# Kernel tuning notes

Measured on AMD Instinct MI355X. Metric: run time of the kernel, lower is better.

Reference implementation:

```python
import jax, jax.numpy as jnp
import numpy as np

B, C, H, W = 8, 512, 96, 96
CQ = 64  # in_places // scale
EPS = 1e-06


def setup_inputs() -> dict:
    key = jax.random.key(0)
    ks = jax.random.split(key, 4)
    x = jax.random.normal(ks[0], (B, C, H, W), dtype=jnp.float32)
    wq = jax.random.normal(ks[1], (CQ, C), dtype=jnp.float32) * (1.0 / np.sqrt(C))
    wk = jax.random.normal(ks[2], (CQ, C), dtype=jnp.float32) * (1.0 / np.sqrt(C))
    wv = jax.random.normal(ks[3], (C, C), dtype=jnp.float32) * (1.0 / np.sqrt(C))
    bq = jnp.zeros((CQ,), jnp.float32)
    bk = jnp.zeros((CQ,), jnp.float32)
    bv = jnp.zeros((C,), jnp.float32)
    gamma = jnp.ones((1,), jnp.float32)
    return {"x": x, "wq": wq, "bq": bq, "wk": wk, "bk": bk, "wv": wv, "bv": bv, "gamma": gamma}


def reference(x, wq, bq, wk, bk, wv, bv, gamma):
    b, c, h, w = x.shape
    n = h * w
    xf = x.reshape(b, c, n)  # [b, c, n]
    # 1x1 convs == per-position channel GEMMs
    Q = jnp.einsum('oc,bcn->bon', wq, xf) + bq[None, :, None]  # [b, cq, n]
    K = jnp.einsum('oc,bcn->bon', wk, xf) + bk[None, :, None]  # [b, cq, n]
    V = jnp.einsum('oc,bcn->bon', wv, xf) + bv[None, :, None]  # [b, c, n]
    # L2 normalize over channel dim (dim=-2), matching torch l2_norm (no eps)
    Q = Q / jnp.linalg.norm(Q, axis=1, keepdims=True)
    K = K / jnp.linalg.norm(K, axis=1, keepdims=True)
    Qt = jnp.transpose(Q, (0, 2, 1))  # [b, n, cq]
    # tailor_sum = 1 / (N + Q . (sum_n K + eps))
    k_sum = K.sum(axis=-1) + EPS  # [b, cq]
    tailor = 1.0 / (n + jnp.einsum('bnm,bm->bn', Qt, k_sum))  # [b, n]
    v_sum = V.sum(axis=-1)  # [b, c]
    matrix = jnp.einsum('bmn,bcn->bmc', K, V)  # [b, cq, c]
    matrix_sum = v_sum[:, :, None] + jnp.einsum('bnm,bmc->bcn', Qt, matrix)  # [b, c, n]
    weight_value = matrix_sum * tailor[:, None, :]  # [b, c, n]
    return x + gamma[0] * weight_value.reshape(b, c, h, w)
```

## Files before the change

### kernel.cpp

```cpp
#include <hip/hip_runtime.h>

#define NB 8
#define NC 512
#define NQ 64
#define NN 9216
#define FEPS 1e-6f

typedef __attribute__((ext_vector_type(8))) short s16x8;
typedef __attribute__((ext_vector_type(4))) float f32x4;

static const size_t OFF_Q    = 0;
static const size_t OFF_KT   = OFF_Q + (size_t)NB * NQ * NN;
static const size_t OFF_KSUM = OFF_KT + (size_t)NB * NQ * NN;
static const size_t OFF_XSUM = OFF_KSUM + (size_t)NB * NQ;
static const size_t OFF_M1   = OFF_XSUM + (size_t)NB * NC;
static const size_t OFF_M2   = OFF_M1 + (size_t)NB * NQ * NC;
static const size_t OFF_VSUM = OFF_M2 + (size_t)NB * NQ * NC;
static const size_t OFF_WB   = OFF_VSUM + (size_t)NB * NC;

__device__ __forceinline__ void load_lds16(const void* g, void* l) {
    __builtin_amdgcn_global_load_lds((const __attribute__((address_space(1))) void*)g,
                                     (__attribute__((address_space(3))) void*)l, 16, 0, 0);
}

__device__ __forceinline__ unsigned cvt_pk_bf16(float lo, float hi) {
    unsigned r;
    asm("v_cvt_pk_bf16_f32 %0, %1, %2" : "=v"(r) : "v"(lo), "v"(hi));
    return r;
}

__device__ __forceinline__ unsigned short f2bf(float f) {
    union { float f; unsigned u; } a; a.f = f;
    unsigned r = a.u + 0x7FFFu + ((a.u >> 16) & 1u);
    return (unsigned short)(r >> 16);
}

__global__ void prep_w_kernel(const float* __restrict__ wq, const float* __restrict__ wk,
                              unsigned short* __restrict__ Wb) {
    const int idx = blockIdx.x * 256 + threadIdx.x;
#pragma unroll
    for (int k = 0; k < 4; ++k) {
        const int f4 = idx + k * 4096;
        const float* src = (f4 < 8192) ? wq : wk;
        const float4 v = *(const float4*)&src[(size_t)(f4 & 8191) * 4];
        uint2 u;
        u.x = cvt_pk_bf16(v.x, v.y);
        u.y = cvt_pk_bf16(v.z, v.w);
        *(uint2*)&Wb[(size_t)f4 * 4] = u;
    }
}

__launch_bounds__(256, 3)
__global__ void qk_mfma_kernel(const float* __restrict__ x,
                               const unsigned short* __restrict__ Wb,
                               const float* __restrict__ bq, const float* __restrict__ bk,
                               unsigned short* __restrict__ Qtb, unsigned short* __restrict__ Ktb,
                               float* __restrict__ ksum) {
    __shared__ __align__(16) unsigned short WX[12672];
    __shared__ float ssqL[4][64];
    unsigned short* Ws = WX;
    unsigned short* Xs = WX + 8192;
    const int t = threadIdx.x;
    const int w = t >> 6, lane = t & 63;
    const int g = lane >> 4, i16 = lane & 15;
    const int b = blockIdx.y;
    const int n0 = blockIdx.x * 64;
    const int srow = (w << 3) + (lane >> 3);
    const int sslot = lane & 7;

    f32x4 acc[2][4];
#pragma unroll
    for (int rt = 0; rt < 2; ++rt)
#pragma unroll
        for (int ct = 0; ct < 4; ++ct) acc[rt][ct] = {0.f, 0.f, 0.f, 0.f};

#pragma unroll 1
    for (int kc = 0; kc < NC; kc += 64) {
#pragma unroll
        for (int q = 0; q < 4; ++q) {
            const int row = q * 32 + srow;
            load_lds16(Wb + (size_t)row * NC + kc + ((sslot ^ (row & 7)) << 3),
                       Ws + (q * 32 + (w << 3)) * 64);
        }
#pragma unroll
        for (int r = 0; r < 2; ++r) {
            const int idx = r * 256 + t;
            const int cp = idx >> 4;
            const int p4 = (idx & 15) << 2;
            const float* xp = &x[((size_t)b * NC + kc + 2 * cp) * NN + n0 + p4];
            const float4 v0 = *(const float4*)xp;
            const float4 v1 = *(const float4*)(xp + NN);
            const float* f0 = (const float*)&v0;
            const float* f1 = (const float*)&v1;
#pragma unroll
            for (int j = 0; j < 4; ++j) {
                const int pos = p4 + j;
                const unsigned u = cvt_pk_bf16(f0[j], f1[j]);
                *(unsigned*)&Xs[pos * 64 + ((2 * cp) ^ ((pos & 7) << 3))] = u;
            }
        }
        __syncthreads();
#pragma unroll
        for (int ks = 0; ks < 2; ++ks) {
            s16x8 af[2], bfr[4];
#pragma unroll
            for (int rt = 0; rt < 2; ++rt) {
                const int row = (w << 5) + (rt << 4) + i16;
                af[rt] = *(const s16x8*)&Ws[row * 64 + (((ks << 5) + (g << 3)) ^ ((row & 7) << 3))];
            }
#pragma unroll
            for (int ct = 0; ct < 4; ++ct) {
                const int row = (ct << 4) + i16;
                bfr[ct] = *(const s16x8*)&Xs[row * 64 + (((ks << 5) + (g << 3)) ^ ((row & 7) << 3))];
            }
#pragma unroll
            for (int rt = 0; rt < 2; ++rt)
#pragma unroll
                for (int ct = 0; ct < 4; ++ct)
                    acc[rt][ct] = __builtin_amdgcn_mfma_f32_16x16x32_bf16(af[rt], bfr[ct], acc[rt][ct], 0, 0, 0);
        }
        __syncthreads();
    }

    const bool isK = (w >= 2);
    const int obase = (w & 1) * 32;
    const float* bias = isK ? bk : bq;
    float bv[2][4];
#pragma unroll
    for (int rt = 0; rt < 2; ++rt)
#pragma unroll
        for (int reg = 0; reg < 4; ++reg)
            bv[rt][reg] = bias[obase + rt * 16 + 4 * g + reg];
#pragma unroll
    for (int rt = 0; rt < 2; ++rt)
#pragma unroll
        for (int ct = 0; ct < 4; ++ct)
#pragma unroll
            for (int reg = 0; reg < 4; ++reg) acc[rt][ct][reg] += bv[rt][reg];

    float sq[4];
#pragma unroll
    for (int ct = 0; ct < 4; ++ct) {
        float s = 0.f;
#pragma unroll
        for (int rt = 0; rt < 2; ++rt)
#pragma unroll
            for (int reg = 0; reg < 4; ++reg) s += acc[rt][ct][reg] * acc[rt][ct][reg];
        s += __shfl_xor(s, 16, 64);
        s += __shfl_xor(s, 32, 64);
        sq[ct] = s;
    }
    ssqL[w][lane] = sq[g];
    __syncthreads();
    const int pairw = (w >> 1) << 1;
    float inv[4];
#pragma unroll
    for (int ct = 0; ct < 4; ++ct) {
        const int p = ct * 16 + i16;
        inv[ct] = rsqrtf(ssqL[pairw][p] + ssqL[pairw + 1][p]);
    }
#pragma unroll
    for (int rt = 0; rt < 2; ++rt)
#pragma unroll
        for (int ct = 0; ct < 4; ++ct)
#pragma unroll
            for (int reg = 0; reg < 4; ++reg) acc[rt][ct][reg] *= inv[ct];

    unsigned short* epQb = WX;
    unsigned short* epK = WX + 8320;
    if (!isK) {
#pragma unroll
        for (int rt = 0; rt < 2; ++rt)
#pragma unroll
            for (int ct = 0; ct < 4; ++ct)
#pragma unroll
                for (int reg = 0; reg < 4; ++reg) {
                    const int o = w * 32 + rt * 16 + 4 * g + reg;
                    const int pos = ct * 16 + i16;
                    epQb[pos * 64 + (o ^ ((pos & 7) << 3))] = f2bf(acc[rt][ct][reg]);
                }
    } else {
#pragma unroll
        for (int rt = 0; rt < 2; ++rt)
#pragma unroll
            for (int reg = 0; reg < 4; ++reg) {
                float s = acc[rt][0][reg] + acc[rt][1][reg] + acc[rt][2][reg] + acc[rt][3][reg];
                s += __shfl_xor(s, 1, 64);
                s += __shfl_xor(s, 2, 64);
                s += __shfl_xor(s, 4, 64);
                s += __shfl_xor(s, 8, 64);
                if (i16 == 0) atomicAdd(&ksum[b * NQ + obase + rt * 16 + 4 * g + reg], s);
            }
#pragma unroll
        for (int rt = 0; rt < 2; ++rt)
#pragma unroll
            for (int ct = 0; ct < 4; ++ct)
#pragma unroll
                for (int reg = 0; reg < 4; ++reg)
                    epK[(obase + rt * 16 + 4 * g + reg) * 68 + ct * 16 + i16] = f2bf(acc[rt][ct][reg]);
    }
    __syncthreads();
    {
        const size_t base = ((size_t)b * NN + n0) * 64;
        const uint4* src = (const uint4*)epQb;
#pragma unroll
        for (int r = 0; r < 2; ++r) {
            const int idx = r * 256 + t;
            *(uint4*)&Qtb[base + (size_t)idx * 8] = src[idx];
        }
    }
#pragma unroll
    for (int r = 0; r < 2; ++r) {
        const int idx = r * 256 + t;
        const int o = idx >> 3, s8 = (idx & 7) * 8;
        uint4 pk;
        unsigned short* up = (unsigned short*)&pk;
#pragma unroll
        for (int j = 0; j < 8; ++j) up[j] = epK[o * 68 + s8 + j];
        *(uint4*)&Ktb[((size_t)b * NQ + o) * NN + n0 + s8] = pk;
    }
}

__launch_bounds__(256, 4)
__global__ void kxt_mfma_kernel(const float* __restrict__ x, const unsigned short* __restrict__ Ktb,
                                float* __restrict__ mat1, float* __restrict__ xsum) {
    __shared__ __align__(16) unsigned short Ks[64 * 64];
    __shared__ __align__(16) unsigned short Xs[64 * 64];
    const int t = threadIdx.x;
    const int w = t >> 6, lane = t & 63;
    const int g = lane >> 4, i16 = lane & 15;
    const int nch = blockIdx.x, ct0 = blockIdx.y, b = blockIdx.z;
    const int c0 = ct0 * 64;
    const int pbeg = nch * 576;
    const int srow = (w << 3) + (lane >> 3);
    const int sslot = lane & 7;

    f32x4 acc[4];
#pragma unroll
    for (int ct = 0; ct < 4; ++ct) acc[ct] = {0.f, 0.f, 0.f, 0.f};
    float xs4[4] = {0.f, 0.f, 0.f, 0.f};

#pragma unroll 1
    for (int p0 = pbeg; p0 < pbeg + 576; p0 += 64) {
#pragma unroll
        for (int q = 0; q < 2; ++q) {
            const int row = q * 32 + srow;
            load_lds16(Ktb + ((size_t)b * NQ + row) * NN + p0 + ((sslot ^ (row & 7)) << 3),
                       Ks + (q * 32 + (w << 3)) * 64);
        }
#pragma unroll
        for (int r = 0; r < 4; ++r) {
            const int idx = r * 256 + t;
            const int c = idx >> 4, n4 = (idx & 15) << 2;
            const float4 v = *(const float4*)&x[((size_t)b * NC + c0 + c) * NN + p0 + n4];
            xs4[r] += (v.x + v.y) + (v.z + v.w);
            uint2 u;
            u.x = cvt_pk_bf16(v.x, v.y);
            u.y = cvt_pk_bf16(v.z, v.w);
            *(uint2*)&Xs[c * 64 + (n4 ^ ((c & 7) << 3))] = u;
        }
        __syncthreads();
#pragma unroll
        for (int ks = 0; ks < 2; ++ks) {
            s16x8 a8, b8[4];
            {
                const int row = (w << 4) + i16;
                a8 = *(const s16x8*)&Ks[row * 64 + (((ks << 5) + (g << 3)) ^ ((row & 7) << 3))];
            }
#pragma unroll
            for (int ct = 0; ct < 4; ++ct) {
                const int row = (ct << 4) + i16;
                b8[ct] = *(const s16x8*)&Xs[row * 64 + (((ks << 5) + (g << 3)) ^ ((row & 7) << 3))];
            }
#pragma unroll
            for (int ct = 0; ct < 4; ++ct)
                acc[ct] = __builtin_amdgcn_mfma_f32_16x16x32_bf16(a8, b8[ct], acc[ct], 0, 0, 0);
        }
        __syncthreads();
    }
    const int ob = (w << 4) + 4 * g;
#pragma unroll
    for (int ct = 0; ct < 4; ++ct)
#pragma unroll
        for (int reg = 0; reg < 4; ++reg)
            atomicAdd(&mat1[((size_t)b * NQ + ob + reg) * NC + c0 + (ct << 4) + i16], acc[ct][reg]);
#pragma unroll
    for (int r = 0; r < 4; ++r) {
        float s = xs4[r];
        s += __shfl_xor(s, 1, 64);
        s += __shfl_xor(s, 2, 64);
        s += __shfl_xor(s, 4, 64);
        s += __shfl_xor(s, 8, 64);
        if (i16 == 0) atomicAdd(&xsum[b * NC + c0 + r * 16 + (t >> 4)], s);
    }
}

__launch_bounds__(256)
__global__ void mat2_kernel(const float* __restrict__ wv, const float* __restrict__ bv,
                            const float* __restrict__ mat1, const float* __restrict__ ksum,
                            const float* __restrict__ xsum,
                            unsigned short* __restrict__ m2bT, float* __restrict__ vsum) {
    __shared__ __align__(16) float m1s[64 * 68];
    __shared__ __align__(16) float wvs[64 * 68];
    const int t = threadIdx.x;
    const int tx = t & 15, ty = t >> 4;
    const int ct = blockIdx.x, b = blockIdx.y;
    const int co0 = ct * 64;
    if (t < 64) {
        const int co = co0 + t;
        float s = 0.f;
        for (int c = 0; c < NC; ++c) s += wv[(size_t)co * NC + c] * xsum[b * NC + c];
        vsum[b * NC + co] = s + (float)NN * bv[co];
    }
    float acc[4][4] = {{0.f}};
    for (int cc = 0; cc < NC; cc += 64) {
#pragma unroll 1
        for (int r = 0; r < 4; ++r) {
            const int idx = r * 256 + t;
            const int row = idx >> 4, a = (idx & 15) * 4;
            *(float4*)&m1s[row * 68 + a] = *(const float4*)&mat1[((size_t)b * NQ + row) * NC + cc + a];
            *(float4*)&wvs[row * 68 + a] = *(const float4*)&wv[(size_t)(co0 + row) * NC + cc + a];
        }
        __syncthreads();
#pragma unroll 8
        for (int c4 = 0; c4 < 16; ++c4) {
            float4 mr[4], wr[4];
#pragma unroll
            for (int jo = 0; jo < 4; ++jo) mr[jo] = *(const float4*)&m1s[(ty + 16 * jo) * 68 + c4 * 4];
#pragma unroll
            for (int jc = 0; jc < 4; ++jc) wr[jc] = *(const float4*)&wvs[(tx + 16 * jc) * 68 + c4 * 4];
#pragma unroll
            for (int jo = 0; jo < 4; ++jo)
#pragma unroll
                for (int jc = 0; jc < 4; ++jc)
                    acc[jo][jc] += mr[jo].x * wr[jc].x + mr[jo].y * wr[jc].y +
                                   mr[jo].z * wr[jc].z + mr[jo].w * wr[jc].w;
        }
        __syncthreads();
    }
#pragma unroll
    for (int jo = 0; jo < 4; ++jo) {
        const float ks = ksum[b * NQ + ty + 16 * jo];
        const int o = ty + 16 * jo;
#pragma unroll
        for (int jc = 0; jc < 4; ++jc) {
            const int co = co0 + tx + 16 * jc;
            m2bT[((size_t)b * NC + co) * NQ + (o ^ ((co & 7) << 3))] = f2bf(acc[jo][jc] + ks * bv[co]);
        }
    }
}

__launch_bounds__(256, 4)
__global__ void final_mfma_kernel(const float* __restrict__ x, const unsigned short* __restrict__ Qtb,
                                  const float* __restrict__ ksum, const unsigned short* __restrict__ m2bT,
                                  const float* __restrict__ vsum, const float* __restrict__ gamma,
                                  float* __restrict__ out) {
    __shared__ __align__(16) unsigned short Qs[64 * 64];
    __shared__ __align__(16) unsigned short Ms[2][64 * 64];
    __shared__ float vsall[512];
    __shared__ float ksl[64];
    __shared__ float tl[64];
    const int t = threadIdx.x;
    const int w = t >> 6, lane = t & 63;
    const int g = lane >> 4, i16 = lane & 15;
    const int b = blockIdx.y;
    const int n0 = blockIdx.x * 64;

    const unsigned short* qg = Qtb + ((size_t)b * NN + n0) * 64;
    const unsigned short* mg = m2bT + (size_t)b * NC * 64;
#pragma unroll
    for (int r = 0; r < 2; ++r) {
        const int off = (w * 2 + r) * 512;
        load_lds16(qg + off + lane * 8, Qs + off);
        load_lds16(mg + off + lane * 8, &Ms[0][off]);
    }
    vsall[t] = vsum[b * NC + t];
    vsall[256 + t] = vsum[b * NC + 256 + t];
    if (t < 64) ksl[t] = ksum[b * NQ + t] + FEPS;
    __syncthreads();
    if (t < 64) {
        float s = 0.f;
        const int sw = (t & 7) << 3;
#pragma unroll 8
        for (int o = 0; o < 64; ++o) {
            union { unsigned u; float f; } cv;
            cv.u = (unsigned)Qs[t * 64 + o] << 16;
            s += cv.f * ksl[o ^ sw];
        }
        tl[t] = 1.0f / ((float)NN + s);
    }
    s16x8 af[4][2];
#pragma unroll
    for (int mt = 0; mt < 4; ++mt)
#pragma unroll
        for (int ks = 0; ks < 2; ++ks) {
            const int row = mt * 16 + i16;
            af[mt][ks] = *(const s16x8*)&Qs[row * 64 + (((ks << 5) + (g << 3)) ^ ((row & 7) << 3))];
        }
    const float gm = gamma[0];
    const int c_local = w * 16 + i16;
    __syncthreads();

#pragma unroll 1
    for (int cc8 = 0; cc8 < 8; ++cc8) {
        if (cc8 < 7) {
#pragma unroll
            for (int r = 0; r < 2; ++r) {
                const int off = (w * 2 + r) * 512;
                load_lds16(mg + (cc8 + 1) * 4096 + off + lane * 8, &Ms[(cc8 + 1) & 1][off]);
            }
        }
        const unsigned short* mbuf = Ms[cc8 & 1];
        s16x8 b8[2];
#pragma unroll
        for (int ks = 0; ks < 2; ++ks)
            b8[ks] = *(const s16x8*)&mbuf[c_local * 64 + (((ks << 5) + (g << 3)) ^ ((i16 & 7) << 3))];
        f32x4 acc[4];
#pragma unroll
        for (int mt = 0; mt < 4; ++mt) acc[mt] = {0.f, 0.f, 0.f, 0.f};
#pragma unroll
        for (int ks = 0; ks < 2; ++ks)
#pragma unroll
            for (int mt = 0; mt < 4; ++mt)
                acc[mt] = __builtin_amdgcn_mfma_f32_16x16x32_bf16(af[mt][ks], b8[ks], acc[mt], 0, 0, 0);
        const int c = cc8 * 64 + c_local;
        const float vsv = vsall[c];
        const size_t rowbase = ((size_t)b * NC + c) * NN + n0;
#pragma unroll
        for (int mt = 0; mt < 4; ++mt) {
            const int p = mt * 16 + 4 * g;
            const float4 xv = *(const float4*)&x[rowbase + p];
            const float4 t4 = *(const float4*)&tl[p];
            float4 ov;
            ov.x = xv.x + gm * (vsv + acc[mt][0]) * t4.x;
            ov.y = xv.y + gm * (vsv + acc[mt][1]) * t4.y;
            ov.z = xv.z + gm * (vsv + acc[mt][2]) * t4.z;
            ov.w = xv.w + gm * (vsv + acc[mt][3]) * t4.w;
            *(float4*)&out[rowbase + p] = ov;
        }
        __syncthreads();
    }
}

extern "C" void kernel_launch(void* const* d_in, const int* in_sizes, int n_in,
                              void* d_out, int out_size, void* d_ws, size_t ws_size,
                              hipStream_t stream) {
    (void)in_sizes; (void)n_in; (void)out_size; (void)ws_size;
    const float* x     = (const float*)d_in[0];
    const float* wq    = (const float*)d_in[1];
    const float* bq    = (const float*)d_in[2];
    const float* wk    = (const float*)d_in[3];
    const float* bk    = (const float*)d_in[4];
    const float* wv    = (const float*)d_in[5];
    const float* bv    = (const float*)d_in[6];
    const float* gamma = (const float*)d_in[7];
    float* out = (float*)d_out;
    float* ws  = (float*)d_ws;

    unsigned short* Qtb  = (unsigned short*)(ws + OFF_Q);
    unsigned short* Ktb  = (unsigned short*)(ws + OFF_KT);
    float* ksum          = ws + OFF_KSUM;
    float* xsum          = ws + OFF_XSUM;
    float* m1            = ws + OFF_M1;
    unsigned short* m2b  = (unsigned short*)(ws + OFF_M2);
    float* vsum          = ws + OFF_VSUM;
    unsigned short* Wb   = (unsigned short*)(ws + OFF_WB);

    hipMemsetAsync(ksum, 0, (size_t)(NB * NQ + NB * NC + NB * NQ * NC) * sizeof(float), stream);

    prep_w_kernel<<<dim3(16), 256, 0, stream>>>(wq, wk, Wb);
    qk_mfma_kernel<<<dim3(NN / 64, NB), 256, 0, stream>>>(x, Wb, bq, bk, Qtb, Ktb, ksum);
    kxt_mfma_kernel<<<dim3(16, 8, NB), 256, 0, stream>>>(x, Ktb, m1, xsum);
    mat2_kernel<<<dim3(8, NB), 256, 0, stream>>>(wv, bv, m1, ksum, xsum, m2b, vsum);
    final_mfma_kernel<<<dim3(NN / 64, NB), 256, 0, stream>>>(x, Qtb, ksum, m2b, vsum, gamma, out);
}
```

Baseline: 436.7 us.

## Fuse K^T·X product into QK kernel and use MFMA for Wv·mat1

The K·Xᵀ accumulation (mat1) and the x channel sums move into the QK projection kernel. Each block multiplies its freshly normalized K tile, kept in LDS, against bf16-converted x tiles and atomically adds the result into mat1, so the Ktb round trip through global memory and the separate kxt kernel go away. The mat2 GEMM is rewritten to use bf16 MFMA with Wv pre-converted to bf16 in the prep kernel. The cost is a second full read of x inside the QK kernel and far more global atomics on mat1, one set per 64-position block instead of per 576-position chunk, which may cause contention.

```diff
diff --git a/kernel.cpp b/kernel.cpp
--- a/kernel.cpp
+++ b/kernel.cpp
@@ -36,17 +36,31 @@
 }
 
 __global__ void prep_w_kernel(const float* __restrict__ wq, const float* __restrict__ wk,
-                              unsigned short* __restrict__ Wb) {
-    const int idx = blockIdx.x * 256 + threadIdx.x;
-#pragma unroll
-    for (int k = 0; k < 4; ++k) {
-        const int f4 = idx + k * 4096;
-        const float* src = (f4 < 8192) ? wq : wk;
-        const float4 v = *(const float4*)&src[(size_t)(f4 & 8191) * 4];
-        uint2 u;
-        u.x = cvt_pk_bf16(v.x, v.y);
-        u.y = cvt_pk_bf16(v.z, v.w);
-        *(uint2*)&Wb[(size_t)f4 * 4] = u;
+                              const float* __restrict__ wv,
+                              unsigned short* __restrict__ Wb, unsigned short* __restrict__ Wvb) {
+    if (blockIdx.x < 16) {
+        const int idx = blockIdx.x * 256 + threadIdx.x;
+#pragma unroll
+        for (int k = 0; k < 4; ++k) {
+            const int f4 = idx + k * 4096;
+            const float* src = (f4 < 8192) ? wq : wk;
+            const float4 v = *(const float4*)&src[(size_t)(f4 & 8191) * 4];
+            uint2 u;
+            u.x = cvt_pk_bf16(v.x, v.y);
+            u.y = cvt_pk_bf16(v.z, v.w);
+            *(uint2*)&Wb[(size_t)f4 * 4] = u;
+        }
+    } else {
+        const int idx = (blockIdx.x - 16) * 256 + threadIdx.x;
+#pragma unroll
+        for (int k = 0; k < 4; ++k) {
+            const int f4 = idx + k * 16384;
+            const float4 v = *(const float4*)&wv[(size_t)f4 * 4];
+            uint2 u;
+            u.x = cvt_pk_bf16(v.x, v.y);
+            u.y = cvt_pk_bf16(v.z, v.w);
+            *(uint2*)&Wvb[(size_t)f4 * 4] = u;
+        }
     }
 }
 
@@ -54,8 +68,9 @@
 __global__ void qk_mfma_kernel(const float* __restrict__ x,
                                const unsigned short* __restrict__ Wb,
                                const float* __restrict__ bq, const float* __restrict__ bk,
-                               unsigned short* __restrict__ Qtb, unsigned short* __restrict__ Ktb,
-                               float* __restrict__ ksum) {
+                               unsigned short* __restrict__ Qtb,
+                               float* __restrict__ ksum, float* __restrict__ xsum,
+                               float* __restrict__ mat1) {
     __shared__ __align__(16) unsigned short WX[12672];
     __shared__ float ssqL[4][64];
     unsigned short* Ws = WX;
@@ -167,7 +182,8 @@
             for (int reg = 0; reg < 4; ++reg) acc[rt][ct][reg] *= inv[ct];
 
     unsigned short* epQb = WX;
-    unsigned short* epK = WX + 8320;
+    unsigned short* epK  = WX + 8192;
+    unsigned short* xb   = WX + 4096;
     if (!isK) {
 #pragma unroll
         for (int rt = 0; rt < 2; ++rt)
@@ -196,8 +212,11 @@
 #pragma unroll
             for (int ct = 0; ct < 4; ++ct)
 #pragma unroll
-                for (int reg = 0; reg < 4; ++reg)
-                    epK[(obase + rt * 16 + 4 * g + reg) * 68 + ct * 16 + i16] = f2bf(acc[rt][ct][reg]);
+                for (int reg = 0; reg < 4; ++reg) {
+                    const int o = obase + rt * 16 + 4 * g + reg;
+                    const int pos = ct * 16 + i16;
+                    epK[o * 64 + (pos ^ ((o & 7) << 3))] = f2bf(acc[rt][ct][reg]);
+                }
     }
     __syncthreads();
     {
@@ -209,145 +228,137 @@
             *(uint4*)&Qtb[base + (size_t)idx * 8] = src[idx];
         }
     }
-#pragma unroll
-    for (int r = 0; r < 2; ++r) {
-        const int idx = r * 256 + t;
-        const int o = idx >> 3, s8 = (idx & 7) * 8;
-        uint4 pk;
-        unsigned short* up = (unsigned short*)&pk;
-#pragma unroll
-        for (int j = 0; j < 8; ++j) up[j] = epK[o * 68 + s8 + j];
-        *(uint4*)&Ktb[((size_t)b * NQ + o) * NN + n0 + s8] = pk;
+
+#pragma unroll 1
+    for (int cc = 0; cc < 8; ++cc) {
+        float xpart[2];
+#pragma unroll
+        for (int r = 0; r < 2; ++r) {
+            const int sg = r * 256 + t;
+            const int c = sg >> 3, s = sg & 7;
+            const float* xp = &x[((size_t)b * NC + cc * 64 + c) * NN + n0 + s * 8];
+            const float4 v0 = *(const float4*)xp;
+            const float4 v1 = *(const float4*)(xp + 4);
+            xpart[r] = (v0.x + v0.y) + (v0.z + v0.w) + (v1.x + v1.y) + (v1.z + v1.w);
+            uint4 u;
+            u.x = cvt_pk_bf16(v0.x, v0.y);
+            u.y = cvt_pk_bf16(v0.z, v0.w);
+            u.z = cvt_pk_bf16(v1.x, v1.y);
+            u.w = cvt_pk_bf16(v1.z, v1.w);
+            *(uint4*)&xb[c * 64 + ((s ^ (c & 7)) << 3)] = u;
+        }
+#pragma unroll
+        for (int r = 0; r < 2; ++r) {
+            float sv = xpart[r];
+            sv += __shfl_xor(sv, 1, 64);
+            sv += __shfl_xor(sv, 2, 64);
+            sv += __shfl_xor(sv, 4, 64);
+            if ((t & 7) == 0) atomicAdd(&xsum[b * NC + cc * 64 + ((r * 256 + t) >> 3)], sv);
+        }
+        __syncthreads();
+        f32x4 macc[4];
+#pragma unroll
+        for (int ct = 0; ct < 4; ++ct) macc[ct] = {0.f, 0.f, 0.f, 0.f};
+#pragma unroll
+        for (int ks = 0; ks < 2; ++ks) {
+            const int arow = (w << 4) + i16;
+            const s16x8 a8 = *(const s16x8*)&epK[arow * 64 + (((ks << 5) + (g << 3)) ^ ((arow & 7) << 3))];
+#pragma unroll
+            for (int ct = 0; ct < 4; ++ct) {
+                const int crow = (ct << 4) + i16;
+                const s16x8 b8 = *(const s16x8*)&xb[crow * 64 + (((ks << 5) + (g << 3)) ^ ((crow & 7) << 3))];
+                macc[ct] = __builtin_amdgcn_mfma_f32_16x16x32_bf16(a8, b8, macc[ct], 0, 0, 0);
+            }
+        }
+        const int ob = (w << 4) + 4 * g;
+#pragma unroll
+        for (int ct = 0; ct < 4; ++ct)
+#pragma unroll
+            for (int reg = 0; reg < 4; ++reg)
+                atomicAdd(&mat1[((size_t)b * NQ + ob + reg) * NC + cc * 64 + (ct << 4) + i16], macc[ct][reg]);
+        __syncthreads();
     }
 }
 
 __launch_bounds__(256, 4)
-__global__ void kxt_mfma_kernel(const float* __restrict__ x, const unsigned short* __restrict__ Ktb,
-                                float* __restrict__ mat1, float* __restrict__ xsum) {
-    __shared__ __align__(16) unsigned short Ks[64 * 64];
-    __shared__ __align__(16) unsigned short Xs[64 * 64];
+__global__ void mat2_mfma_kernel(const float* __restrict__ wv, const float* __restrict__ bv,
+                                 const unsigned short* __restrict__ Wvb,
+                                 const float* __restrict__ mat1, const float* __restrict__ ksum,
+                                 const float* __restrict__ xsum,
+                                 unsigned short* __restrict__ m2bT, float* __restrict__ vsum) {
+    __shared__ __align__(16) unsigned short m1b[64 * 64];
+    __shared__ __align__(16) unsigned short wvs[64 * 64];
+    __shared__ float xsl[512];
     const int t = threadIdx.x;
     const int w = t >> 6, lane = t & 63;
     const int g = lane >> 4, i16 = lane & 15;
-    const int nch = blockIdx.x, ct0 = blockIdx.y, b = blockIdx.z;
-    const int c0 = ct0 * 64;
-    const int pbeg = nch * 576;
+    const int cot = blockIdx.x, b = blockIdx.y;
+    const int co0 = cot * 64;
     const int srow = (w << 3) + (lane >> 3);
     const int sslot = lane & 7;
+    xsl[t] = xsum[b * NC + t];
+    xsl[256 + t] = xsum[b * NC + 256 + t];
 
     f32x4 acc[4];
 #pragma unroll
     for (int ct = 0; ct < 4; ++ct) acc[ct] = {0.f, 0.f, 0.f, 0.f};
-    float xs4[4] = {0.f, 0.f, 0.f, 0.f};
 
 #pragma unroll 1
-    for (int p0 = pbeg; p0 < pbeg + 576; p0 += 64) {
+    for (int cc = 0; cc < NC; cc += 64) {
 #pragma unroll
         for (int q = 0; q < 2; ++q) {
             const int row = q * 32 + srow;
-            load_lds16(Ktb + ((size_t)b * NQ + row) * NN + p0 + ((sslot ^ (row & 7)) << 3),
-                       Ks + (q * 32 + (w << 3)) * 64);
-        }
-#pragma unroll
-        for (int r = 0; r < 4; ++r) {
-            const int idx = r * 256 + t;
-            const int c = idx >> 4, n4 = (idx & 15) << 2;
-            const float4 v = *(const float4*)&x[((size_t)b * NC + c0 + c) * NN + p0 + n4];
-            xs4[r] += (v.x + v.y) + (v.z + v.w);
-            uint2 u;
-            u.x = cvt_pk_bf16(v.x, v.y);
-            u.y = cvt_pk_bf16(v.z, v.w);
-            *(uint2*)&Xs[c * 64 + (n4 ^ ((c & 7) << 3))] = u;
+            load_lds16(Wvb + (size_t)(co0 + row) * NC + cc + ((sslot ^ (row & 7)) << 3),
+                       wvs + (q * 32 + (w << 3)) * 64);
+        }
+#pragma unroll
+        for (int r = 0; r < 2; ++r) {
+            const int sg = r * 256 + t;
+            const int o = sg >> 3, s = sg & 7;
+            const float* mp = &mat1[((size_t)b * NQ + o) * NC + cc + s * 8];
+            const float4 v0 = *(const float4*)mp;
+            const float4 v1 = *(const float4*)(mp + 4);
+            uint4 u;
+            u.x = cvt_pk_bf16(v0.x, v0.y);
+            u.y = cvt_pk_bf16(v0.z, v0.w);
+            u.z = cvt_pk_bf16(v1.x, v1.y);
+            u.w = cvt_pk_bf16(v1.z, v1.w);
+            *(uint4*)&m1b[o * 64 + ((s ^ (o & 7)) << 3)] = u;
         }
         __syncthreads();
 #pragma unroll
         for (int ks = 0; ks < 2; ++ks) {
-            s16x8 a8, b8[4];
-            {
-                const int row = (w << 4) + i16;
-                a8 = *(const s16x8*)&Ks[row * 64 + (((ks << 5) + (g << 3)) ^ ((row & 7) << 3))];
-            }
+            const int arow = (w << 4) + i16;
+            const s16x8 a8 = *(const s16x8*)&m1b[arow * 64 + (((ks << 5) + (g << 3)) ^ ((arow & 7) << 3))];
 #pragma unroll
             for (int ct = 0; ct < 4; ++ct) {
-                const int row = (ct << 4) + i16;
-                b8[ct] = *(const s16x8*)&Xs[row * 64 + (((ks << 5) + (g << 3)) ^ ((row & 7) << 3))];
-            }
-#pragma unroll
-            for (int ct = 0; ct < 4; ++ct)
-                acc[ct] = __builtin_amdgcn_mfma_f32_16x16x32_bf16(a8, b8[ct], acc[ct], 0, 0, 0);
-        }
-        __syncthreads();
-    }
-    const int ob = (w << 4) + 4 * g;
-#pragma unroll
-    for (int ct = 0; ct < 4; ++ct)
-#pragma unroll
-        for (int reg = 0; reg < 4; ++reg)
-            atomicAdd(&mat1[((size_t)b * NQ + ob + reg) * NC + c0 + (ct << 4) + i16], acc[ct][reg]);
-#pragma unroll
-    for (int r = 0; r < 4; ++r) {
-        float s = xs4[r];
+                const int brow = (ct << 4) + i16;
+                const s16x8 b8 = *(const s16x8*)&wvs[brow * 64 + (((ks << 5) + (g << 3)) ^ ((brow & 7) << 3))];
+                acc[ct] = __builtin_amdgcn_mfma_f32_16x16x32_bf16(a8, b8, acc[ct], 0, 0, 0);
+            }
+        }
+        __syncthreads();
+    }
+    {
+        const int co_l = t >> 2, p = t & 3;
+        const float* wp = &wv[(size_t)(co0 + co_l) * NC + p * 128];
+        float s = 0.f;
+#pragma unroll 4
+        for (int i = 0; i < 128; ++i) s += wp[i] * xsl[p * 128 + i];
         s += __shfl_xor(s, 1, 64);
         s += __shfl_xor(s, 2, 64);
-        s += __shfl_xor(s, 4, 64);
-        s += __shfl_xor(s, 8, 64);
-        if (i16 == 0) atomicAdd(&xsum[b * NC + c0 + r * 16 + (t >> 4)], s);
-    }
-}
-
-__launch_bounds__(256)
-__global__ void mat2_kernel(const float* __restrict__ wv, const float* __restrict__ bv,
-                            const float* __restrict__ mat1, const float* __restrict__ ksum,
-                            const float* __restrict__ xsum,
-                            unsigned short* __restrict__ m2bT, float* __restrict__ vsum) {
-    __shared__ __align__(16) float m1s[64 * 68];
-    __shared__ __align__(16) float wvs[64 * 68];
-    const int t = threadIdx.x;
-    const int tx = t & 15, ty = t >> 4;
-    const int ct = blockIdx.x, b = blockIdx.y;
-    const int co0 = ct * 64;
-    if (t < 64) {
-        const int co = co0 + t;
-        float s = 0.f;
-        for (int c = 0; c < NC; ++c) s += wv[(size_t)co * NC + c] * xsum[b * NC + c];
-        vsum[b * NC + co] = s + (float)NN * bv[co];
-    }
-    float acc[4][4] = {{0.f}};
-    for (int cc = 0; cc < NC; cc += 64) {
-#pragma unroll 1
-        for (int r = 0; r < 4; ++r) {
-            const int idx = r * 256 + t;
-            const int row = idx >> 4, a = (idx & 15) * 4;
-            *(float4*)&m1s[row * 68 + a] = *(const float4*)&mat1[((size_t)b * NQ + row) * NC + cc + a];
-            *(float4*)&wvs[row * 68 + a] = *(const float4*)&wv[(size_t)(co0 + row) * NC + cc + a];
-        }
-        __syncthreads();
-#pragma unroll 8
-        for (int c4 = 0; c4 < 16; ++c4) {
-            float4 mr[4], wr[4];
-#pragma unroll
-            for (int jo = 0; jo < 4; ++jo) mr[jo] = *(const float4*)&m1s[(ty + 16 * jo) * 68 + c4 * 4];
-#pragma unroll
-            for (int jc = 0; jc < 4; ++jc) wr[jc] = *(const float4*)&wvs[(tx + 16 * jc) * 68 + c4 * 4];
-#pragma unroll
-            for (int jo = 0; jo < 4; ++jo)
-#pragma unroll
-                for (int jc = 0; jc < 4; ++jc)
-                    acc[jo][jc] += mr[jo].x * wr[jc].x + mr[jo].y * wr[jc].y +
-                                   mr[jo].z * wr[jc].z + mr[jo].w * wr[jc].w;
-        }
-        __syncthreads();
-    }
-#pragma unroll
-    for (int jo = 0; jo < 4; ++jo) {
-        const float ks = ksum[b * NQ + ty + 16 * jo];
-        const int o = ty + 16 * jo;
-#pragma unroll
-        for (int jc = 0; jc < 4; ++jc) {
-            const int co = co0 + tx + 16 * jc;
-            m2bT[((size_t)b * NC + co) * NQ + (o ^ ((co & 7) << 3))] = f2bf(acc[jo][jc] + ks * bv[co]);
-        }
-    }
+        if (p == 0) vsum[b * NC + co0 + co_l] = s + (float)NN * bv[co0 + co_l];
+    }
+    const int ob = (w << 4) + 4 * g;
+#pragma unroll
+    for (int ct = 0; ct < 4; ++ct)
+#pragma unroll
+        for (int reg = 0; reg < 4; ++reg) {
+            const int o = ob + reg;
+            const int co = co0 + (ct << 4) + i16;
+            m2bT[((size_t)b * NC + co) * NQ + (o ^ ((co & 7) << 3))] =
+                f2bf(acc[ct][reg] + ksum[b * NQ + o] * bv[co]);
+        }
 }
 
 __launch_bounds__(256, 4)
@@ -458,7 +469,7 @@
     float* ws  = (float*)d_ws;
 
     unsigned short* Qtb  = (unsigned short*)(ws + OFF_Q);
-    unsigned short* Ktb  = (unsigned short*)(ws + OFF_KT);
+    unsigned short* Wvb  = (unsigned short*)(ws + OFF_KT);
     float* ksum          = ws + OFF_KSUM;
     float* xsum          = ws + OFF_XSUM;
     float* m1            = ws + OFF_M1;
@@ -468,9 +479,8 @@
 
     hipMemsetAsync(ksum, 0, (size_t)(NB * NQ + NB * NC + NB * NQ * NC) * sizeof(float), stream);
 
-    prep_w_kernel<<<dim3(16), 256, 0, stream>>>(wq, wk, Wb);
-    qk_mfma_kernel<<<dim3(NN / 64, NB), 256, 0, stream>>>(x, Wb, bq, bk, Qtb, Ktb, ksum);
-    kxt_mfma_kernel<<<dim3(16, 8, NB), 256, 0, stream>>>(x, Ktb, m1, xsum);
-    mat2_kernel<<<dim3(8, NB), 256, 0, stream>>>(wv, bv, m1, ksum, xsum, m2b, vsum);
+    prep_w_kernel<<<dim3(80), 256, 0, stream>>>(wq, wk, wv, Wb, Wvb);
+    qk_mfma_kernel<<<dim3(NN / 64, NB), 256, 0, stream>>>(x, Wb, bq, bk, Qtb, ksum, xsum, m1);
+    mat2_mfma_kernel<<<dim3(8, NB), 256, 0, stream>>>(wv, bv, Wvb, m1, ksum, xsum, m2b, vsum);
     final_mfma_kernel<<<dim3(NN / 64, NB), 256, 0, stream>>>(x, Qtb, ksum, m2b, vsum, gamma, out);
 }
```

New measurement: 482.1 us. 10.4% more time.
